# Kernel optimization log

Hardware: AMD Instinct MI355X
Metric: run time of the kernel (lower is better)

The kernel has to match this reference:

```python
import jax, jax.numpy as jnp
import numpy as np

IN_FEATURES = 4096
OUT_FEATURES = 11008
PACKED = (IN_FEATURES + 1) // 2  # 2048
B, S = 4, 2048


def setup_inputs() -> dict:
    key = jax.random.key(0)
    k1, k2, k3, k4 = jax.random.split(key, 4)
    x = jax.random.normal(k1, (B, S, IN_FEATURES), dtype=jnp.float32)
    # packed uint8 bytes stored as int32 in [0, 256)
    qweight = jax.random.randint(k2, (OUT_FEATURES, PACKED), 0, 256, dtype=jnp.int32)
    scale = jax.random.uniform(k3, (OUT_FEATURES,), dtype=jnp.float32, minval=0.001, maxval=0.02)
    bias = jax.random.normal(k4, (OUT_FEATURES,), dtype=jnp.float32)
    return {"x": x, "qweight": qweight, "scale": scale, "bias": bias}


def _dequantize(qweight, scale, in_features):
    # unpack two signed int4 nibbles per byte: low = bits 0-3, high = bits 4-7
    low = (qweight & 15) - 8          # [out, packed]
    high = ((qweight >> 4) & 15) - 8  # [out, packed]
    # interleave low/high: column order low0, high0, low1, high1, ...
    q = jnp.stack([low, high], axis=-1).reshape(qweight.shape[0], -1)[:, :in_features]
    return q.astype(jnp.float32) * scale[:, None]  # [out, in]


def reference(x, qweight, scale, bias):
    W = _dequantize(qweight, scale, IN_FEATURES)  # [out, in]
    # F.linear: x @ W.T + bias
    return jnp.einsum('bsi,oi->bso', x, W) + bias
```

## Files before the change

### kernel.cpp

```cpp
#include <hip/hip_runtime.h>


typedef _Float16 half8 __attribute__((ext_vector_type(8)));
typedef float    floatx4 __attribute__((ext_vector_type(4)));
typedef float    fvec4 __attribute__((ext_vector_type(4)));
typedef int      ivec4 __attribute__((ext_vector_type(4)));

constexpr int M_TOT   = 8192;
constexpr int N_TOT   = 11008;
constexpr int K_TOT   = 4096;
constexpr int PACKEDC = 2048;
constexpr int NKT     = K_TOT / 128;
constexpr size_t XQ_BYTES = (size_t)M_TOT * K_TOT;
constexpr size_t SM_BYTES = (size_t)M_TOT * 4;
constexpr size_t WQ_BYTES = (size_t)N_TOT * K_TOT;

#define MEMFENCE() asm volatile("" ::: "memory")
static __device__ __forceinline__ void bar() {
    MEMFENCE(); __builtin_amdgcn_s_barrier(); MEMFENCE();
}

__global__ __launch_bounds__(256)
void quant_x_kernel(const float* __restrict__ x, signed char* __restrict__ xq,
                    float* __restrict__ sm)
{
    const int row = blockIdx.x;
    const int t   = threadIdx.x;
    const float* xr = x + (size_t)row * K_TOT;

    fvec4 v[4];
    #pragma unroll
    for (int k = 0; k < 4; ++k) v[k] = ((const fvec4*)xr)[t + 256 * k];

    float mx = 0.0f;
    #pragma unroll
    for (int k = 0; k < 4; ++k)
        #pragma unroll
        for (int j = 0; j < 4; ++j) mx = fmaxf(mx, __builtin_fabsf(v[k][j]));

    #pragma unroll
    for (int off = 32; off >= 1; off >>= 1) mx = fmaxf(mx, __shfl_xor(mx, off, 64));
    __shared__ float wm[4];
    if ((t & 63) == 0) wm[t >> 6] = mx;
    __syncthreads();
    mx = fmaxf(fmaxf(wm[0], wm[1]), fmaxf(wm[2], wm[3]));
    mx = fmaxf(mx, 1e-20f);
    const float inv = 127.0f / mx;
    if (t == 0) sm[row] = mx / 127.0f;

    signed char* oq = xq + (size_t)row * K_TOT;
    #pragma unroll
    for (int k = 0; k < 4; ++k) {
        unsigned w = 0;
        #pragma unroll
        for (int j = 0; j < 4; ++j) {
            int q = (int)rintf(v[k][j] * inv);
            q = q > 127 ? 127 : (q < -127 ? -127 : q);
            w |= (unsigned)(q & 0xFF) << (8 * j);
        }
        *(unsigned*)(oq + t * 4 + 1024 * k) = w;
    }
}

__global__ void quant_q_kernel(const int* __restrict__ q, signed char* __restrict__ wq, int n8) {
    const int stride = gridDim.x * blockDim.x;
    for (int i = blockIdx.x * blockDim.x + threadIdx.x; i < n8; i += stride) {
        int ow[4];
        #pragma unroll
        for (int h = 0; h < 2; ++h) {
            ivec4 d = ((const ivec4*)q)[2 * i + h];
            #pragma unroll
            for (int e = 0; e < 2; ++e) {
                const int b0 = d[2 * e], b1 = d[2 * e + 1];
                ow[2 * h + e] = (int)( (unsigned)(((b0 & 15) - 8) & 0xFF)
                                     | ((unsigned)((((b0 >> 4) & 15) - 8) & 0xFF) << 8)
                                     | ((unsigned)(((b1 & 15) - 8) & 0xFF) << 16)
                                     | ((unsigned)((((b1 >> 4) & 15) - 8) & 0xFF) << 24));
            }
        }
        *(ivec4*)(wq + (size_t)i * 16) = *(ivec4*)ow;
    }
}

__global__ __launch_bounds__(512, 2)
void gemm8p_i8_kernel(const signed char* __restrict__ A, const signed char* __restrict__ Bm,
                      const float* __restrict__ sm, const float* __restrict__ scale,
                      const float* __restrict__ bias, float* __restrict__ out)
{
    __shared__ signed char L[2][2][2][128 * 128];

    const int tid  = threadIdx.x;
    const int lane = tid & 63;
    const int wave = tid >> 6;
    const int wr   = wave >> 2;
    const int wc   = wave & 3;
    const int fr   = lane & 15;
    const int kg   = lane >> 4;

    const int bid  = blockIdx.x;
    const int swz  = (bid & 7) * 172 + (bid >> 3);
    const int band = swz / 344;
    const int rr   = swz % 344;
    const int tm   = band * 8 + (rr & 7);
    const int tn   = rr >> 3;

    const int srow = lane >> 3;
    const int sg   = lane & 7;
    const int sgk  = sg ^ srow;

    const signed char* Ag = A  + (size_t)(tm * 256) * K_TOT;
    const signed char* Bg = Bm + (size_t)(tn * 256) * K_TOT;

    ivec4 acc[8][4];
    #pragma unroll
    for (int i = 0; i < 8; ++i)
        #pragma unroll
        for (int j = 0; j < 4; ++j)
            acc[i][j] = (ivec4)0;

    auto stage = [&](int slot, int mat, int half, int kt) {
        if (kt >= NKT) kt = NKT - 1;
        const signed char* gb = mat ? Bg : Ag;
        #pragma unroll
        for (int i = 0; i < 2; ++i) {
            const int row = wave * 16 + i * 8 + srow;
            const signed char* g = gb + (size_t)(half * 128 + row) * K_TOT + kt * 128 + sgk * 16;
            signed char* l = &L[slot][mat][half][row * 128 + sg * 16];
            __builtin_amdgcn_global_load_lds((const __attribute__((address_space(1))) void*)g,
                                             (__attribute__((address_space(3))) void*)l, 16, 0, 0);
        }
    };

    ivec4 a0[4][2], a1[4][2], bb[2][2];

    auto ldA = [&](int slot, int mh, ivec4 (&d)[4][2]) {
        const char* base = (const char*)&L[slot][0][wr][0];
        #pragma unroll
        for (int m4 = 0; m4 < 4; ++m4)
            #pragma unroll
            for (int ks = 0; ks < 2; ++ks) {
                const int row = (mh * 4 + m4) * 16 + fr;
                const int off = row * 128 + ((ks * 64 + kg * 16) ^ ((fr & 7) << 4));
                d[m4][ks] = *(const ivec4*)(base + off);
            }
    };
    auto ldB = [&](int slot, int nh) {
        const char* base = (const char*)&L[slot][1][wc >> 1][0];
        #pragma unroll
        for (int n2 = 0; n2 < 2; ++n2)
            #pragma unroll
            for (int ks = 0; ks < 2; ++ks) {
                const int row = (wc & 1) * 64 + (nh * 2 + n2) * 16 + fr;
                const int off = row * 128 + ((ks * 64 + kg * 16) ^ ((fr & 7) << 4));
                bb[n2][ks] = *(const ivec4*)(base + off);
            }
    };
    auto mma = [&](int mh, int nh, ivec4 (&a)[4][2]) {
        __builtin_amdgcn_s_setprio(1);
        #pragma unroll
        for (int m4 = 0; m4 < 4; ++m4)
            #pragma unroll
            for (int n2 = 0; n2 < 2; ++n2)
                #pragma unroll
                for (int ks = 0; ks < 2; ++ks)
                    acc[mh * 4 + m4][nh * 2 + n2] = __builtin_amdgcn_mfma_i32_16x16x64_i8(
                        a[m4][ks], bb[n2][ks], acc[mh * 4 + m4][nh * 2 + n2], 0, 0, 0);
        __builtin_amdgcn_s_setprio(0);
    };

    stage(0, 0, 0, 0); stage(0, 0, 1, 0); stage(0, 1, 0, 0); stage(0, 1, 1, 0);
    stage(1, 0, 0, 1); stage(1, 0, 1, 1);
    asm volatile("s_waitcnt vmcnt(4)" ::: "memory");
    bar();

    #pragma unroll 1
    for (int it = 0; it < K_TOT / 256; ++it) {
        const int t1 = 2 * it + 1, t2 = 2 * it + 2, t3 = 2 * it + 3;
        ldA(0, 0, a0); ldB(0, 0); stage(1, 1, 0, t1);
        asm volatile("s_waitcnt lgkmcnt(8)" ::: "memory");
        bar(); asm volatile("s_waitcnt lgkmcnt(0)" ::: "memory");
        mma(0, 0, a0); bar();
        ldA(0, 1, a1); stage(1, 1, 1, t1);
        bar(); asm volatile("s_waitcnt lgkmcnt(0)" ::: "memory");
        mma(1, 0, a1); bar();
        ldB(0, 1); stage(0, 0, 0, t2);
        bar(); asm volatile("s_waitcnt lgkmcnt(0)" ::: "memory");
        mma(1, 1, a1); bar();
        stage(0, 0, 1, t2);
        bar();
        mma(0, 1, a0);
        asm volatile("s_waitcnt vmcnt(4)" ::: "memory");
        bar();
        ldA(1, 0, a0); ldB(1, 0); stage(0, 1, 0, t2);
        asm volatile("s_waitcnt lgkmcnt(8)" ::: "memory");
        bar(); asm volatile("s_waitcnt lgkmcnt(0)" ::: "memory");
        mma(0, 0, a0); bar();
        ldA(1, 1, a1); stage(0, 1, 1, t2);
        bar(); asm volatile("s_waitcnt lgkmcnt(0)" ::: "memory");
        mma(1, 0, a1); bar();
        ldB(1, 1); stage(1, 0, 0, t3);
        bar(); asm volatile("s_waitcnt lgkmcnt(0)" ::: "memory");
        mma(1, 1, a1); bar();
        stage(1, 0, 1, t3);
        bar();
        mma(0, 1, a0);
        asm volatile("s_waitcnt vmcnt(4)" ::: "memory");
        bar();
    }

    asm volatile("s_waitcnt vmcnt(0)" ::: "memory");

    float srv[8][4];
    const float* smr = sm + tm * 256 + wr * 128 + kg * 4;
    #pragma unroll
    for (int mi = 0; mi < 8; ++mi)
        #pragma unroll
        for (int j = 0; j < 4; ++j)
            srv[mi][j] = smr[mi * 16 + j];

    #pragma unroll
    for (int ni = 0; ni < 4; ++ni) {
        const int col = tn * 256 + wc * 64 + ni * 16 + fr;
        const float s  = scale[col];
        const float bv = bias[col];
        #pragma unroll
        for (int mi = 0; mi < 8; ++mi) {
            const int row0 = tm * 256 + wr * 128 + mi * 16 + kg * 4;
            #pragma unroll
            for (int j = 0; j < 4; ++j)
                __builtin_nontemporal_store((float)acc[mi][ni][j] * (srv[mi][j] * s) + bv,
                                            out + (size_t)(row0 + j) * N_TOT + col);
        }
    }
}

constexpr int LDSS = 40;

__global__ __launch_bounds__(256, 2)
void int4lin_fused_kernel(const float* __restrict__ X,
                          const int*   __restrict__ Q,
                          const float* __restrict__ scale,
                          const float* __restrict__ bias,
                          float*       __restrict__ out)
{
    __shared__ _Float16 As[2][128][LDSS];
    __shared__ _Float16 Bs[2][128][LDSS];

    const int tid  = threadIdx.x;
    const int lane = tid & 63;
    const int bx   = blockIdx.x;
    const int by   = blockIdx.y;
    const int wave = tid >> 6;
    const int wm   = (wave >> 1) * 64;
    const int wn   = (wave & 1) * 64;
    const int fr   = lane & 15;
    const int kg   = lane >> 4;

    const int srow  = tid >> 1;
    const int shalf = tid & 1;

    const float* aptr = X + (size_t)(by * 128 + srow) * K_TOT + shalf * 16;
    const int*   bptr = Q + (size_t)(bx * 128 + srow) * PACKEDC + shalf * 8;

    floatx4 acc[4][4];
    #pragma unroll
    for (int i = 0; i < 4; ++i)
        #pragma unroll
        for (int j = 0; j < 4; ++j)
            acc[i][j] = (floatx4)0.0f;

    fvec4 araw[4];
    ivec4 braw[2];

    auto gload = [&](int kt) {
        const fvec4* ap = (const fvec4*)(aptr + (size_t)kt * 32);
        #pragma unroll
        for (int i = 0; i < 4; ++i) araw[i] = ap[i];
        const ivec4* bp = (const ivec4*)(bptr + kt * 16);
        #pragma unroll
        for (int i = 0; i < 2; ++i) braw[i] = bp[i];
    };

    auto cvt_write = [&](int buf) {
        #pragma unroll
        for (int v = 0; v < 2; ++v) {
            half8 h;
            #pragma unroll
            for (int e = 0; e < 8; ++e)
                h[e] = (_Float16)araw[v * 2 + (e >> 2)][e & 3];
            *(half8*)&As[buf][srow][shalf * 16 + v * 8] = h;
        }
        #pragma unroll
        for (int v = 0; v < 2; ++v) {
            half8 h;
            #pragma unroll
            for (int e = 0; e < 4; ++e) {
                const int b = braw[v][e];
                h[2 * e]     = (_Float16)((b & 15) - 8);
                h[2 * e + 1] = (_Float16)((b >> 4) - 8);
            }
            *(half8*)&Bs[buf][srow][shalf * 16 + v * 8] = h;
        }
    };

    gload(0);
    cvt_write(0);
    __syncthreads();

    int cur = 0;
    #pragma unroll 1
    for (int kt = 0; kt < K_TOT / 32; ++kt) {
        if (kt + 1 < K_TOT / 32) gload(kt + 1);

        half8 af[4], bf[4];
        #pragma unroll
        for (int mi = 0; mi < 4; ++mi)
            af[mi] = *(const half8*)&As[cur][wm + mi * 16 + fr][kg * 8];
        #pragma unroll
        for (int ni = 0; ni < 4; ++ni)
            bf[ni] = *(const half8*)&Bs[cur][wn + ni * 16 + fr][kg * 8];

        #pragma unroll
        for (int mi = 0; mi < 4; ++mi)
            #pragma unroll
            for (int ni = 0; ni < 4; ++ni)
                acc[mi][ni] = __builtin_amdgcn_mfma_f32_16x16x32_f16(
                    af[mi], bf[ni], acc[mi][ni], 0, 0, 0);

        if (kt + 1 < K_TOT / 32) cvt_write(cur ^ 1);
        __syncthreads();
        cur ^= 1;
    }

    #pragma unroll
    for (int ni = 0; ni < 4; ++ni) {
        const int col = bx * 128 + wn + ni * 16 + fr;
        const float s  = scale[col];
        const float bv = bias[col];
        #pragma unroll
        for (int mi = 0; mi < 4; ++mi) {
            const int row0 = by * 128 + wm + mi * 16 + kg * 4;
            #pragma unroll
            for (int j = 0; j < 4; ++j)
                out[(size_t)(row0 + j) * N_TOT + col] = acc[mi][ni][j] * s + bv;
        }
    }
}

extern "C" void kernel_launch(void* const* d_in, const int* in_sizes, int n_in,
                              void* d_out, int out_size, void* d_ws, size_t ws_size,
                              hipStream_t stream) {
    const float* x     = (const float*)d_in[0];
    const int*   q     = (const int*)d_in[1];
    const float* scale = (const float*)d_in[2];
    const float* bias  = (const float*)d_in[3];
    float*       out   = (float*)d_out;

    if (ws_size >= XQ_BYTES + SM_BYTES + WQ_BYTES) {
        signed char* xq = (signed char*)d_ws;
        float*       sm = (float*)((char*)d_ws + XQ_BYTES);
        signed char* wq = (signed char*)((char*)d_ws + XQ_BYTES + SM_BYTES);
        quant_x_kernel<<<M_TOT, 256, 0, stream>>>(x, xq, sm);
        quant_q_kernel<<<2048, 256, 0, stream>>>(q, wq, N_TOT * PACKEDC / 8);
        gemm8p_i8_kernel<<<(M_TOT / 256) * (N_TOT / 256), 512, 0, stream>>>(
            xq, wq, sm, scale, bias, out);
    } else {
        dim3 grid(N_TOT / 128, M_TOT / 128);
        int4lin_fused_kernel<<<grid, dim3(256), 0, stream>>>(x, q, scale, bias, out);
    }
}
```

Before: 426.2 us.

## Double-buffer B fragments and prefetch LDS reads ahead of MFMA blocks

Splits the B register fragment into two buffers and reorders the main loop so each LDS fragment load for the next MFMA sub-block is issued before the current MFMA sub-block. The first A/B fragments of each K-slot are loaded ahead of the loop iteration. This drops the explicit lgkmcnt waits and several barriers so LDS reads overlap matrix-core work. In exchange it uses more registers, which could lower occupancy or cause spills. It also relies on the compiler to place the LDS wait counts correctly.

```diff
diff --git a/kernel.cpp b/kernel.cpp
--- a/kernel.cpp
+++ b/kernel.cpp
@@ -131,7 +131,7 @@
         }
     };
 
-    ivec4 a0[4][2], a1[4][2], bb[2][2];
+    ivec4 a0[4][2], a1[4][2], bb0[2][2], bb1[2][2];
 
     auto ldA = [&](int slot, int mh, ivec4 (&d)[4][2]) {
         const char* base = (const char*)&L[slot][0][wr][0];
@@ -144,7 +144,7 @@
                 d[m4][ks] = *(const ivec4*)(base + off);
             }
     };
-    auto ldB = [&](int slot, int nh) {
+    auto ldB = [&](int slot, int nh, ivec4 (&d)[2][2]) {
         const char* base = (const char*)&L[slot][1][wc >> 1][0];
         #pragma unroll
         for (int n2 = 0; n2 < 2; ++n2)
@@ -152,10 +152,10 @@
             for (int ks = 0; ks < 2; ++ks) {
                 const int row = (wc & 1) * 64 + (nh * 2 + n2) * 16 + fr;
                 const int off = row * 128 + ((ks * 64 + kg * 16) ^ ((fr & 7) << 4));
-                bb[n2][ks] = *(const ivec4*)(base + off);
+                d[n2][ks] = *(const ivec4*)(base + off);
             }
     };
-    auto mma = [&](int mh, int nh, ivec4 (&a)[4][2]) {
+    auto mma = [&](int mh, int nh, ivec4 (&a)[4][2], ivec4 (&b)[2][2]) {
         __builtin_amdgcn_s_setprio(1);
         #pragma unroll
         for (int m4 = 0; m4 < 4; ++m4)
@@ -164,7 +164,7 @@
                 #pragma unroll
                 for (int ks = 0; ks < 2; ++ks)
                     acc[mh * 4 + m4][nh * 2 + n2] = __builtin_amdgcn_mfma_i32_16x16x64_i8(
-                        a[m4][ks], bb[n2][ks], acc[mh * 4 + m4][nh * 2 + n2], 0, 0, 0);
+                        a[m4][ks], b[n2][ks], acc[mh * 4 + m4][nh * 2 + n2], 0, 0, 0);
         __builtin_amdgcn_s_setprio(0);
     };
 
@@ -172,40 +172,45 @@
     stage(1, 0, 0, 1); stage(1, 0, 1, 1);
     asm volatile("s_waitcnt vmcnt(4)" ::: "memory");
     bar();
+    ldA(0, 0, a0); ldB(0, 0, bb0);
 
     #pragma unroll 1
     for (int it = 0; it < K_TOT / 256; ++it) {
         const int t1 = 2 * it + 1, t2 = 2 * it + 2, t3 = 2 * it + 3;
-        ldA(0, 0, a0); ldB(0, 0); stage(1, 1, 0, t1);
-        asm volatile("s_waitcnt lgkmcnt(8)" ::: "memory");
-        bar(); asm volatile("s_waitcnt lgkmcnt(0)" ::: "memory");
-        mma(0, 0, a0); bar();
-        ldA(0, 1, a1); stage(1, 1, 1, t1);
-        bar(); asm volatile("s_waitcnt lgkmcnt(0)" ::: "memory");
-        mma(1, 0, a1); bar();
-        ldB(0, 1); stage(0, 0, 0, t2);
-        bar(); asm volatile("s_waitcnt lgkmcnt(0)" ::: "memory");
-        mma(1, 1, a1); bar();
+        bar();
+        stage(1, 1, 0, t1);
+        ldA(0, 1, a1);
+        mma(0, 0, a0, bb0);
+        bar();
+        stage(1, 1, 1, t1);
+        ldB(0, 1, bb1);
+        mma(1, 0, a1, bb0);
+        bar();
+        stage(0, 0, 0, t2);
+        mma(1, 1, a1, bb1);
+        bar();
         stage(0, 0, 1, t2);
-        bar();
-        mma(0, 1, a0);
+        mma(0, 1, a0, bb1);
         asm volatile("s_waitcnt vmcnt(4)" ::: "memory");
         bar();
-        ldA(1, 0, a0); ldB(1, 0); stage(0, 1, 0, t2);
-        asm volatile("s_waitcnt lgkmcnt(8)" ::: "memory");
-        bar(); asm volatile("s_waitcnt lgkmcnt(0)" ::: "memory");
-        mma(0, 0, a0); bar();
-        ldA(1, 1, a1); stage(0, 1, 1, t2);
-        bar(); asm volatile("s_waitcnt lgkmcnt(0)" ::: "memory");
-        mma(1, 0, a1); bar();
-        ldB(1, 1); stage(1, 0, 0, t3);
-        bar(); asm volatile("s_waitcnt lgkmcnt(0)" ::: "memory");
-        mma(1, 1, a1); bar();
+        ldA(1, 0, a0); ldB(1, 0, bb0);
+        bar();
+        stage(0, 1, 0, t2);
+        ldA(1, 1, a1);
+        mma(0, 0, a0, bb0);
+        bar();
+        stage(0, 1, 1, t2);
+        ldB(1, 1, bb1);
+        mma(1, 0, a1, bb0);
+        bar();
+        stage(1, 0, 0, t3);
+        mma(1, 1, a1, bb1);
+        bar();
         stage(1, 0, 1, t3);
-        bar();
-        mma(0, 1, a0);
+        mma(0, 1, a0, bb1);
         asm volatile("s_waitcnt vmcnt(4)" ::: "memory");
         bar();
+        ldA(0, 0, a0); ldB(0, 0, bb0);
     }
 
     asm volatile("s_waitcnt vmcnt(0)" ::: "memory");
```

Measured after the change: 450.9 us. +5.8%, slower.

## Shrink int8 GEMM tile to 256x64 with higher occupancy

Applied to the files above, without the earlier changes.

The int8 MFMA GEMM block tile changes from 256x256 to 256x64. LDS drops to 80KB (two A slots of 256x128 plus two B slots of 64x128), the wave layout becomes 4x2, and the grid grows fourfold with launch bounds raised to 4 blocks per CU. The goal is better occupancy and load balance, at the cost of lower arithmetic intensity: each byte of A staged in LDS now serves only 64 columns, so A global traffic rises sharply. The LDS sync schedule is reworked, and B is staged with one load per thread.

```diff
diff --git a/kernel.cpp b/kernel.cpp
--- a/kernel.cpp
+++ b/kernel.cpp
@@ -82,126 +82,130 @@
     }
 }
 
-__global__ __launch_bounds__(512, 2)
+__global__ __launch_bounds__(512, 4)
 void gemm8p_i8_kernel(const signed char* __restrict__ A, const signed char* __restrict__ Bm,
                       const float* __restrict__ sm, const float* __restrict__ scale,
                       const float* __restrict__ bias, float* __restrict__ out)
 {
-    __shared__ signed char L[2][2][2][128 * 128];
+    __shared__ signed char LA[2][2][128 * 128];
+    __shared__ signed char LB[2][64 * 128];
 
     const int tid  = threadIdx.x;
     const int lane = tid & 63;
     const int wave = tid >> 6;
-    const int wr   = wave >> 2;
-    const int wc   = wave & 3;
+    const int wr   = wave >> 1;
+    const int wc   = wave & 1;
     const int fr   = lane & 15;
     const int kg   = lane >> 4;
 
     const int bid  = blockIdx.x;
-    const int swz  = (bid & 7) * 172 + (bid >> 3);
-    const int band = swz / 344;
-    const int rr   = swz % 344;
+    const int swz  = (bid & 7) * 688 + (bid >> 3);
+    const int band = swz / 1376;
+    const int rr   = swz % 1376;
     const int tm   = band * 8 + (rr & 7);
     const int tn   = rr >> 3;
 
     const int srow = lane >> 3;
     const int sg   = lane & 7;
     const int sgk  = sg ^ srow;
+    const int browS = tid >> 3;
+    const int sgB  = tid & 7;
+    const int sgkB = sgB ^ (browS & 7);
 
     const signed char* Ag = A  + (size_t)(tm * 256) * K_TOT;
-    const signed char* Bg = Bm + (size_t)(tn * 256) * K_TOT;
-
-    ivec4 acc[8][4];
-    #pragma unroll
-    for (int i = 0; i < 8; ++i)
-        #pragma unroll
-        for (int j = 0; j < 4; ++j)
+    const signed char* Bg = Bm + (size_t)(tn * 64)  * K_TOT;
+
+    ivec4 acc[4][2];
+    #pragma unroll
+    for (int i = 0; i < 4; ++i)
+        #pragma unroll
+        for (int j = 0; j < 2; ++j)
             acc[i][j] = (ivec4)0;
 
-    auto stage = [&](int slot, int mat, int half, int kt) {
+    auto stageA = [&](int slot, int half, int kt) {
         if (kt >= NKT) kt = NKT - 1;
-        const signed char* gb = mat ? Bg : Ag;
         #pragma unroll
         for (int i = 0; i < 2; ++i) {
             const int row = wave * 16 + i * 8 + srow;
-            const signed char* g = gb + (size_t)(half * 128 + row) * K_TOT + kt * 128 + sgk * 16;
-            signed char* l = &L[slot][mat][half][row * 128 + sg * 16];
+            const signed char* g = Ag + (size_t)(half * 128 + row) * K_TOT + kt * 128 + sgk * 16;
+            signed char* l = &LA[slot][half][row * 128 + sg * 16];
             __builtin_amdgcn_global_load_lds((const __attribute__((address_space(1))) void*)g,
                                              (__attribute__((address_space(3))) void*)l, 16, 0, 0);
         }
     };
-
-    ivec4 a0[4][2], a1[4][2], bb[2][2];
-
-    auto ldA = [&](int slot, int mh, ivec4 (&d)[4][2]) {
-        const char* base = (const char*)&L[slot][0][wr][0];
-        #pragma unroll
-        for (int m4 = 0; m4 < 4; ++m4)
+    auto stageB = [&](int slot, int kt) {
+        if (kt >= NKT) kt = NKT - 1;
+        const signed char* g = Bg + (size_t)browS * K_TOT + kt * 128 + sgkB * 16;
+        signed char* l = &LB[slot][browS * 128 + sgB * 16];
+        __builtin_amdgcn_global_load_lds((const __attribute__((address_space(1))) void*)g,
+                                         (__attribute__((address_space(3))) void*)l, 16, 0, 0);
+    };
+
+    ivec4 a0[2][2], a1[2][2], bb[2];
+
+    auto ldA = [&](int slot, int mh, ivec4 (&d)[2][2]) {
+        const char* base = (const char*)&LA[slot][wr >> 1][0];
+        #pragma unroll
+        for (int m2 = 0; m2 < 2; ++m2)
             #pragma unroll
             for (int ks = 0; ks < 2; ++ks) {
-                const int row = (mh * 4 + m4) * 16 + fr;
+                const int row = (wr & 1) * 64 + (mh * 2 + m2) * 16 + fr;
                 const int off = row * 128 + ((ks * 64 + kg * 16) ^ ((fr & 7) << 4));
-                d[m4][ks] = *(const ivec4*)(base + off);
+                d[m2][ks] = *(const ivec4*)(base + off);
             }
     };
     auto ldB = [&](int slot, int nh) {
-        const char* base = (const char*)&L[slot][1][wc >> 1][0];
-        #pragma unroll
-        for (int n2 = 0; n2 < 2; ++n2)
-            #pragma unroll
-            for (int ks = 0; ks < 2; ++ks) {
-                const int row = (wc & 1) * 64 + (nh * 2 + n2) * 16 + fr;
-                const int off = row * 128 + ((ks * 64 + kg * 16) ^ ((fr & 7) << 4));
-                bb[n2][ks] = *(const ivec4*)(base + off);
-            }
-    };
-    auto mma = [&](int mh, int nh, ivec4 (&a)[4][2]) {
+        const char* base = (const char*)&LB[slot][0];
+        #pragma unroll
+        for (int ks = 0; ks < 2; ++ks) {
+            const int row = wc * 32 + nh * 16 + fr;
+            const int off = row * 128 + ((ks * 64 + kg * 16) ^ ((fr & 7) << 4));
+            bb[ks] = *(const ivec4*)(base + off);
+        }
+    };
+    auto mma = [&](int mh, int nh, ivec4 (&a)[2][2]) {
         __builtin_amdgcn_s_setprio(1);
         #pragma unroll
-        for (int m4 = 0; m4 < 4; ++m4)
-            #pragma unroll
-            for (int n2 = 0; n2 < 2; ++n2)
-                #pragma unroll
-                for (int ks = 0; ks < 2; ++ks)
-                    acc[mh * 4 + m4][nh * 2 + n2] = __builtin_amdgcn_mfma_i32_16x16x64_i8(
-                        a[m4][ks], bb[n2][ks], acc[mh * 4 + m4][nh * 2 + n2], 0, 0, 0);
+        for (int m2 = 0; m2 < 2; ++m2)
+            #pragma unroll
+            for (int ks = 0; ks < 2; ++ks)
+                acc[mh * 2 + m2][nh] = __builtin_amdgcn_mfma_i32_16x16x64_i8(
+                    a[m2][ks], bb[ks], acc[mh * 2 + m2][nh], 0, 0, 0);
         __builtin_amdgcn_s_setprio(0);
     };
 
-    stage(0, 0, 0, 0); stage(0, 0, 1, 0); stage(0, 1, 0, 0); stage(0, 1, 1, 0);
-    stage(1, 0, 0, 1); stage(1, 0, 1, 1);
+    stageA(0, 0, 0); stageA(0, 1, 0); stageB(0, 0);
+    stageA(1, 0, 1); stageA(1, 1, 1);
     asm volatile("s_waitcnt vmcnt(4)" ::: "memory");
     bar();
 
     #pragma unroll 1
     for (int it = 0; it < K_TOT / 256; ++it) {
         const int t1 = 2 * it + 1, t2 = 2 * it + 2, t3 = 2 * it + 3;
-        ldA(0, 0, a0); ldB(0, 0); stage(1, 1, 0, t1);
-        asm volatile("s_waitcnt lgkmcnt(8)" ::: "memory");
+        ldA(0, 0, a0); ldB(0, 0); stageB(1, t1);
         bar(); asm volatile("s_waitcnt lgkmcnt(0)" ::: "memory");
         mma(0, 0, a0); bar();
-        ldA(0, 1, a1); stage(1, 1, 1, t1);
+        ldA(0, 1, a1);
         bar(); asm volatile("s_waitcnt lgkmcnt(0)" ::: "memory");
         mma(1, 0, a1); bar();
-        ldB(0, 1); stage(0, 0, 0, t2);
+        ldB(0, 1); stageA(0, 0, t2);
         bar(); asm volatile("s_waitcnt lgkmcnt(0)" ::: "memory");
         mma(1, 1, a1); bar();
-        stage(0, 0, 1, t2);
+        stageA(0, 1, t2);
         bar();
         mma(0, 1, a0);
         asm volatile("s_waitcnt vmcnt(4)" ::: "memory");
         bar();
-        ldA(1, 0, a0); ldB(1, 0); stage(0, 1, 0, t2);
-        asm volatile("s_waitcnt lgkmcnt(8)" ::: "memory");
+        ldA(1, 0, a0); ldB(1, 0); stageB(0, t2);
         bar(); asm volatile("s_waitcnt lgkmcnt(0)" ::: "memory");
         mma(0, 0, a0); bar();
-        ldA(1, 1, a1); stage(0, 1, 1, t2);
+        ldA(1, 1, a1);
         bar(); asm volatile("s_waitcnt lgkmcnt(0)" ::: "memory");
         mma(1, 0, a1); bar();
-        ldB(1, 1); stage(1, 0, 0, t3);
+        ldB(1, 1); stageA(1, 0, t3);
         bar(); asm volatile("s_waitcnt lgkmcnt(0)" ::: "memory");
         mma(1, 1, a1); bar();
-        stage(1, 0, 1, t3);
+        stageA(1, 1, t3);
         bar();
         mma(0, 1, a0);
         asm volatile("s_waitcnt vmcnt(4)" ::: "memory");
@@ -210,22 +214,22 @@
 
     asm volatile("s_waitcnt vmcnt(0)" ::: "memory");
 
-    float srv[8][4];
-    const float* smr = sm + tm * 256 + wr * 128 + kg * 4;
-    #pragma unroll
-    for (int mi = 0; mi < 8; ++mi)
+    float srv[4][4];
+    const float* smr = sm + tm * 256 + wr * 64 + kg * 4;
+    #pragma unroll
+    for (int mi = 0; mi < 4; ++mi)
         #pragma unroll
         for (int j = 0; j < 4; ++j)
             srv[mi][j] = smr[mi * 16 + j];
 
     #pragma unroll
-    for (int ni = 0; ni < 4; ++ni) {
-        const int col = tn * 256 + wc * 64 + ni * 16 + fr;
+    for (int ni = 0; ni < 2; ++ni) {
+        const int col = tn * 64 + wc * 32 + ni * 16 + fr;
         const float s  = scale[col];
         const float bv = bias[col];
         #pragma unroll
-        for (int mi = 0; mi < 8; ++mi) {
-            const int row0 = tm * 256 + wr * 128 + mi * 16 + kg * 4;
+        for (int mi = 0; mi < 4; ++mi) {
+            const int row0 = tm * 256 + wr * 64 + mi * 16 + kg * 4;
             #pragma unroll
             for (int j = 0; j < 4; ++j)
                 __builtin_nontemporal_store((float)acc[mi][ni][j] * (srv[mi][j] * s) + bv,
@@ -362,7 +366,7 @@
         signed char* wq = (signed char*)((char*)d_ws + XQ_BYTES + SM_BYTES);
         quant_x_kernel<<<M_TOT, 256, 0, stream>>>(x, xq, sm);
         quant_q_kernel<<<2048, 256, 0, stream>>>(q, wq, N_TOT * PACKEDC / 8);
-        gemm8p_i8_kernel<<<(M_TOT / 256) * (N_TOT / 256), 512, 0, stream>>>(
+        gemm8p_i8_kernel<<<(M_TOT / 256) * (N_TOT / 64), 512, 0, stream>>>(
             xq, wq, sm, scale, bias, out);
     } else {
         dim3 grid(N_TOT / 128, M_TOT / 128);
```

Result: slower. 510.8 us (+19.8%).
